# Kernel optimization log

Measured on AMD Instinct MI355X. Metric: run time of the kernel, lower is better.

Reference implementation:

```python
import jax, jax.numpy as jnp
import numpy as np

N, E, G = 50000, 800000, 256
H, C = 8, 16
F0 = 64
FH = H * C  # 128
L = 6
EPS = 1e-5
SEL = [0, 1, 2, 3, 4, 5, 5, 5]  # <10 layers -> pad with last


def setup_inputs() -> dict:
    key = jax.random.key(0)
    ks = jax.random.split(key, 32)

    def w(k, shape, fan_in):
        return jax.random.normal(k, shape, jnp.float32) / np.float32(np.sqrt(fan_in))

    inp = {
        'x': jax.random.normal(ks[0], (N, F0), jnp.float32),
        'edge_index': jax.random.randint(ks[1], (2, E), 0, N),
        'batch_vec': jnp.sort(jax.random.randint(ks[2], (N,), 0, G)),
        # layer 0 (in=F0)
        'Wq0': w(ks[3], (F0, FH), F0), 'bq0': 0.01 * jax.random.normal(ks[4], (FH,), jnp.float32),
        'Wk0': w(ks[5], (F0, FH), F0), 'bk0': 0.01 * jax.random.normal(ks[6], (FH,), jnp.float32),
        'Wv0': w(ks[7], (F0, FH), F0), 'bv0': 0.01 * jax.random.normal(ks[8], (FH,), jnp.float32),
        'Ws0': w(ks[9], (F0, FH), F0), 'bs0': 0.01 * jax.random.normal(ks[10], (FH,), jnp.float32),
        # layers 1..L-1 (in=FH), stacked
        'Wq': w(ks[11], (L - 1, FH, FH), FH), 'bq': 0.01 * jax.random.normal(ks[12], (L - 1, FH), jnp.float32),
        'Wk': w(ks[13], (L - 1, FH, FH), FH), 'bk': 0.01 * jax.random.normal(ks[14], (L - 1, FH), jnp.float32),
        'Wv': w(ks[15], (L - 1, FH, FH), FH), 'bv': 0.01 * jax.random.normal(ks[16], (L - 1, FH), jnp.float32),
        'Ws': w(ks[17], (L - 1, FH, FH), FH), 'bs': 0.01 * jax.random.normal(ks[18], (L - 1, FH), jnp.float32),
        # BatchNorm affine params per layer
        'gamma': jnp.ones((L, FH), jnp.float32),
        'beta': jnp.zeros((L, FH), jnp.float32),
    }
    return inp


def _transformer_conv(x, src, dst, Wq, bq, Wk, bk, Wv, bv, Ws, bs):
    # q from target nodes, k/v from source nodes (PyG TransformerConv, concat=True)
    q = (x @ Wq + bq).reshape(-1, H, C)
    k = (x @ Wk + bk).reshape(-1, H, C)
    v = (x @ Wv + bv).reshape(-1, H, C)
    s = jnp.einsum('ehc,ehc->eh', q[dst], k[src]) * np.float32(1.0 / np.sqrt(C))  # [E,H]
    m = jax.ops.segment_max(s, dst, num_segments=N)       # segment softmax over in-edges
    e = jnp.exp(s - m[dst])
    denom = jax.ops.segment_sum(e, dst, num_segments=N)
    alpha = e / jnp.maximum(denom[dst], 1e-16)            # [E,H]
    msg = jax.ops.segment_sum(alpha[:, :, None] * v[src], dst, num_segments=N)  # [N,H,C]
    return msg.reshape(-1, FH) + (x @ Ws + bs)            # root/skip connection


def _bn_relu(x, g, b):
    mu = jnp.mean(x, axis=0)
    var = jnp.var(x, axis=0)  # biased, as used for normalization in training mode
    return jax.nn.relu((x - mu) * jax.lax.rsqrt(var + EPS) * g + b)


def reference(x, edge_index, batch_vec, Wq0, bq0, Wk0, bk0, Wv0, bv0, Ws0, bs0,
              Wq, bq, Wk, bk, Wv, bv, Ws, bs, gamma, beta):
    src, dst = edge_index[0], edge_index[1]
    outs = []
    h = _bn_relu(_transformer_conv(x, src, dst, Wq0, bq0, Wk0, bk0, Wv0, bv0, Ws0, bs0),
                 gamma[0], beta[0])
    outs.append(h)
    for i in range(L - 1):
        h = _bn_relu(_transformer_conv(h, src, dst, Wq[i], bq[i], Wk[i], bk[i],
                                       Wv[i], bv[i], Ws[i], bs[i]),
                     gamma[i + 1], beta[i + 1])
        outs.append(h)
    counts = jnp.maximum(jax.ops.segment_sum(jnp.ones((N,), x.dtype), batch_vec, num_segments=G), 1.0)
    pooled = [jax.ops.segment_sum(o, batch_vec, num_segments=G) / counts[:, None] for o in outs]
    latent = jnp.stack([pooled[i] for i in SEL], axis=1)  # [G, 8, FH]
    return latent.reshape(G, -1)                          # [G, 8*FH]
```

## Files before the change

kernel.cpp:

```cpp
#include <hip/hip_runtime.h>
#include <hip/hip_bf16.h>
#include <math.h>

#define NN 50000
#define NE 800000
#define NG 256
#define FHH 128
#define NL 6
#define NCH 49
#define NB 391

typedef __attribute__((ext_vector_type(8))) short s16x8;
typedef __attribute__((ext_vector_type(4))) float f32x4;

#define QSCALE 0.36067376022224085f

__device__ __forceinline__ ushort f2bf(float x) {
  uint u = __float_as_uint(x);
  u += 0x7fffu + ((u >> 16) & 1u);
  return (ushort)(u >> 16);
}
__device__ __forceinline__ float bf2f(ushort h) {
  return __uint_as_float(((uint)h) << 16);
}
__device__ __forceinline__ float bfl(uint u) { return __uint_as_float(u << 16); }
__device__ __forceinline__ float bfh(uint u) { return __uint_as_float(u & 0xffff0000u); }
__device__ __forceinline__ uint packbf(float a, float b) {
  return (uint)f2bf(a) | ((uint)f2bf(b) << 16);
}

__device__ __forceinline__ void gload16(const ushort* g, ushort* l) {
  __builtin_amdgcn_global_load_lds(
      (const __attribute__((address_space(1))) uint*)(const void*)g,
      (__attribute__((address_space(3))) uint*)(void*)l, 16, 0, 0);
}

__global__ void k_gstart(const int* __restrict__ bv, int* __restrict__ gstart) {
  int g = blockIdx.x * blockDim.x + threadIdx.x;
  if (g > NG) return;
  int lo = 0, hi = NN;
  while (lo < hi) { int mid = (lo + hi) >> 1; if (bv[mid] < g) lo = mid + 1; else hi = mid; }
  gstart[g] = lo;
}

__global__ void k_deg(const int* __restrict__ dstv, int* __restrict__ deg) {
  int e = blockIdx.x * blockDim.x + threadIdx.x;
  if (e < NE) atomicAdd(&deg[dstv[e]], 1);
}

__global__ __launch_bounds__(256) void k_scanA(const int* __restrict__ deg, int* __restrict__ part) {
  int b = blockIdx.x, t = threadIdx.x;
  int s = 0;
  for (int j = t; j < 1024; j += 256) { int i = b * 1024 + j; if (i < NN) s += deg[i]; }
  __shared__ int sh[4];
  for (int o = 32; o; o >>= 1) s += __shfl_down(s, o, 64);
  if ((t & 63) == 0) sh[t >> 6] = s;
  __syncthreads();
  if (t == 0) part[b] = sh[0] + sh[1] + sh[2] + sh[3];
}

__global__ void k_scanB(int* __restrict__ part, int* __restrict__ row_ptr) {
  if (threadIdx.x == 0 && blockIdx.x == 0) {
    int run = 0;
    for (int i = 0; i < NCH; ++i) { int v = part[i]; part[i] = run; run += v; }
    row_ptr[NN] = run;
  }
}

__global__ __launch_bounds__(1024) void k_scanC(const int* __restrict__ deg, const int* __restrict__ part,
                                                int* __restrict__ row_ptr, int* __restrict__ cursor) {
  __shared__ int buf[1024];
  int b = blockIdx.x, t = threadIdx.x;
  int i = b * 1024 + t;
  int v = (i < NN) ? deg[i] : 0;
  buf[t] = v;
  __syncthreads();
  for (int off = 1; off < 1024; off <<= 1) {
    int add = (t >= off) ? buf[t - off] : 0;
    __syncthreads();
    buf[t] += add;
    __syncthreads();
  }
  if (i < NN) { int ex = part[b] + buf[t] - v; row_ptr[i] = ex; cursor[i] = ex; }
}

__global__ void k_scatter(const int* __restrict__ srcv, const int* __restrict__ dstv,
                          int* __restrict__ cursor, uint* __restrict__ colb) {
  int e = blockIdx.x * blockDim.x + threadIdx.x;
  if (e < NE) {
    int d = dstv[e];
    int pos = atomicAdd(&cursor[d], 1);
    colb[pos] = ((uint)srcv[e]) << 9;
  }
}

__device__ __forceinline__ size_t wtile_idx(int k, int c) {
  return (size_t)(k >> 5) * 4096 + ((((c >> 4) * 4 + ((k & 31) >> 3)) * 16 + (c & 15)) * 8 + (k & 7));
}

__global__ __launch_bounds__(256) void k_wconv0(const float* __restrict__ W0, const float* __restrict__ W1,
                                                const float* __restrict__ W2, const float* __restrict__ W3,
                                                ushort* __restrict__ wh, ushort* __restrict__ wl) {
  int id = blockIdx.x * 256 + threadIdx.x;
  if (id >= 4 * 64 * 128) return;
  int mat = id >> 13, rem = id & 8191;
  int k = rem >> 7, c = rem & 127;
  const float* W = (mat == 0) ? W0 : (mat == 1) ? W1 : (mat == 2) ? W2 : W3;
  float v = W[k * 128 + c];
  ushort h = f2bf(v);
  ushort lo = f2bf(v - bf2f(h));
  size_t dst = (size_t)mat * 8192 + wtile_idx(k, c);
  wh[dst] = h; wl[dst] = lo;
}

__global__ __launch_bounds__(256) void k_wconvS(const float* __restrict__ Wq, const float* __restrict__ Wk,
                                                const float* __restrict__ Wv, const float* __restrict__ Ws,
                                                ushort* __restrict__ wh, ushort* __restrict__ wl) {
  int id = blockIdx.x * 256 + threadIdx.x;
  if (id >= 5 * 4 * 16384) return;
  int lay = id / 65536, rem = id % 65536;
  int mat = rem >> 14, rem2 = rem & 16383;
  int k = rem2 >> 7, c = rem2 & 127;
  const float* W = (mat == 0) ? Wq : (mat == 1) ? Wk : (mat == 2) ? Wv : Ws;
  float v = W[(size_t)lay * 16384 + k * 128 + c];
  ushort h = f2bf(v);
  ushort lo = f2bf(v - bf2f(h));
  size_t dst = 32768 + ((size_t)lay * 4 + mat) * 16384 + wtile_idx(k, c);
  wh[dst] = h; wl[dst] = lo;
}

template <int K>
__global__ __launch_bounds__(256) void k_presplit(const float* __restrict__ Y,
                                                  ushort* __restrict__ Xh, ushort* __restrict__ Xl) {
  const int CP = K / 4;
  int idx = blockIdx.x * 256 + threadIdx.x;
  int row = idx / CP;
  int c4 = (idx % CP) * 4;
  if (row >= NN) return;
  float4 v = *reinterpret_cast<const float4*>(Y + (size_t)row * K + c4);
  ushort h0 = f2bf(v.x), h1 = f2bf(v.y), h2 = f2bf(v.z), h3 = f2bf(v.w);
  ushort l0 = f2bf(v.x - bf2f(h0)), l1 = f2bf(v.y - bf2f(h1));
  ushort l2 = f2bf(v.z - bf2f(h2)), l3 = f2bf(v.w - bf2f(h3));
  int b = row >> 7, g = (row & 127) >> 4, frow = row & 15;
  int ks = c4 >> 5, qq = (c4 & 31) >> 3, j = c4 & 7;
  size_t base = ((size_t)ks * NB + b) * 4096 + (((g * 4 + qq) * 16) + frow) * 8 + j;
  *reinterpret_cast<uint2*>(Xh + base) =
      make_uint2((uint)h0 | ((uint)h1 << 16), (uint)h2 | ((uint)h3 << 16));
  *reinterpret_cast<uint2*>(Xl + base) =
      make_uint2((uint)l0 | ((uint)l1 << 16), (uint)l2 | ((uint)l3 << 16));
}

template <int K>
__global__ __launch_bounds__(256, 2) void k_gemm(
    const ushort* __restrict__ Xh, const ushort* __restrict__ Xl,
    const ushort* __restrict__ Wth, const ushort* __restrict__ Wtl,
    const float* __restrict__ b0, const float* __restrict__ b1,
    const float* __restrict__ b2, const float* __restrict__ b3,
    ushort* __restrict__ qbf, ushort* __restrict__ kv, float* __restrict__ Yxs) {
  __shared__ __align__(16) ushort Ah[4096];
  __shared__ __align__(16) ushort Al[4096];
  __shared__ __align__(16) ushort Bh[4096];
  __shared__ __align__(16) ushort Bl[4096];
  int bid = blockIdx.x;
  int mat = (bid >> 3) & 3;
  int b = (bid & 7) + ((bid >> 5) << 3);
  if (b >= NB) return;
  int t = threadIdx.x;
  int lane = t & 63, w = t >> 6;
  int wr = w >> 1, wc = w & 1;
  int frow = lane & 15;
  const ushort* wh = Wth + (size_t)mat * (K * 128);
  const ushort* wl = Wtl + (size_t)mat * (K * 128);
  const float* bb = (mat == 0) ? b0 : (mat == 1) ? b1 : (mat == 2) ? b2 : b3;

  f32x4 acc[4][4];
#pragma unroll
  for (int i = 0; i < 4; ++i)
#pragma unroll
    for (int j = 0; j < 4; ++j)
#pragma unroll
      for (int r = 0; r < 4; ++r) acc[i][j][r] = 0.f;

  int wofs = w * 1024 + lane * 8;
  for (int ks = 0; ks < K / 32; ++ks) {
    size_t abase = ((size_t)ks * NB + b) * 4096;
    const ushort* gAh = Xh + abase + wofs;
    const ushort* gAl = Xl + abase + wofs;
    const ushort* gBh = wh + ks * 4096 + wofs;
    const ushort* gBl = wl + ks * 4096 + wofs;
    gload16(gAh, &Ah[w * 1024]);
    gload16(gAh + 512, &Ah[w * 1024 + 512]);
    gload16(gAl, &Al[w * 1024]);
    gload16(gAl + 512, &Al[w * 1024 + 512]);
    gload16(gBh, &Bh[w * 1024]);
    gload16(gBh + 512, &Bh[w * 1024 + 512]);
    gload16(gBl, &Bl[w * 1024]);
    gload16(gBl + 512, &Bl[w * 1024 + 512]);
    __syncthreads();
    s16x8 ah[4], al[4], bh[4], bl[4];
#pragma unroll
    for (int g = 0; g < 4; ++g) {
      ah[g] = *reinterpret_cast<const s16x8*>(&Ah[(wr * 4 + g) * 512 + lane * 8]);
      al[g] = *reinterpret_cast<const s16x8*>(&Al[(wr * 4 + g) * 512 + lane * 8]);
      bh[g] = *reinterpret_cast<const s16x8*>(&Bh[(wc * 4 + g) * 512 + lane * 8]);
      bl[g] = *reinterpret_cast<const s16x8*>(&Bl[(wc * 4 + g) * 512 + lane * 8]);
    }
#pragma unroll
    for (int rg = 0; rg < 4; ++rg)
#pragma unroll
      for (int cg = 0; cg < 4; ++cg) {
        acc[rg][cg] = __builtin_amdgcn_mfma_f32_16x16x32_bf16(ah[rg], bh[cg], acc[rg][cg], 0, 0, 0);
        acc[rg][cg] = __builtin_amdgcn_mfma_f32_16x16x32_bf16(al[rg], bh[cg], acc[rg][cg], 0, 0, 0);
        acc[rg][cg] = __builtin_amdgcn_mfma_f32_16x16x32_bf16(ah[rg], bl[cg], acc[rg][cg], 0, 0, 0);
      }
    __syncthreads();
  }
  int r0 = b * 128;
  int qq = (lane >> 4) << 2;
#pragma unroll
  for (int rg = 0; rg < 4; ++rg) {
#pragma unroll
    for (int cg = 0; cg < 4; ++cg) {
      int colg = wc * 64 + cg * 16 + frow;
      float bv = bb[colg];
#pragma unroll
      for (int r = 0; r < 4; ++r) {
        int row = r0 + wr * 64 + rg * 16 + qq + r;
        if (row >= NN) continue;
        float val = acc[rg][cg][r] + bv;
        if (mat == 0)      qbf[(size_t)row * FHH + colg] = f2bf(val * QSCALE);
        else if (mat == 3) Yxs[(size_t)row * FHH + colg] = val;
        else {
          int pos = (colg >> 1) * 4 + ((mat == 2) ? 2 : 0) + (colg & 1);
          kv[(size_t)row * 256 + pos] = f2bf(val);
        }
      }
    }
  }
}

__global__ __launch_bounds__(256) void k_agg(const uint* __restrict__ qb,
                                             const ushort* __restrict__ kv,
                                             const float* __restrict__ xs,
                                             const int* __restrict__ row_ptr,
                                             const uint* __restrict__ colb,
                                             uint* __restrict__ yb) {
  int n = blockIdx.x * 4 + (threadIdx.x >> 6);
  int t = threadIdx.x & 63;
  uint qp = qb[(n << 6) + t];
  float qx = bfl(qp), qy = bfh(qp);
  const char* kvb = (const char*)kv;
  uint tof = (uint)t * 8u;
  int e0 = row_ptr[n], e1 = row_ptr[n + 1];
  float sum = 0.f, a0 = 0.f, a1 = 0.f;
  int i = e0;
  for (; i + 4 <= e1; i += 4) {
    uint o0 = colb[i] + tof, o1 = colb[i + 1] + tof;
    uint o2 = colb[i + 2] + tof, o3 = colb[i + 3] + tof;
    uint2 d0 = *(const uint2*)(kvb + o0);
    uint2 d1 = *(const uint2*)(kvb + o1);
    uint2 d2 = *(const uint2*)(kvb + o2);
    uint2 d3 = *(const uint2*)(kvb + o3);
    float p0 = fmaf(qx, bfl(d0.x), qy * bfh(d0.x));
    float p1 = fmaf(qx, bfl(d1.x), qy * bfh(d1.x));
    float p2 = fmaf(qx, bfl(d2.x), qy * bfh(d2.x));
    float p3 = fmaf(qx, bfl(d3.x), qy * bfh(d3.x));
    p0 += __shfl_xor(p0, 1, 8); p1 += __shfl_xor(p1, 1, 8);
    p2 += __shfl_xor(p2, 1, 8); p3 += __shfl_xor(p3, 1, 8);
    p0 += __shfl_xor(p0, 2, 8); p1 += __shfl_xor(p1, 2, 8);
    p2 += __shfl_xor(p2, 2, 8); p3 += __shfl_xor(p3, 2, 8);
    p0 += __shfl_xor(p0, 4, 8); p1 += __shfl_xor(p1, 4, 8);
    p2 += __shfl_xor(p2, 4, 8); p3 += __shfl_xor(p3, 4, 8);
    float w0 = exp2f(fminf(p0, 110.f));
    float w1 = exp2f(fminf(p1, 110.f));
    float w2 = exp2f(fminf(p2, 110.f));
    float w3 = exp2f(fminf(p3, 110.f));
    sum += (w0 + w1) + (w2 + w3);
    a0 = fmaf(w0, bfl(d0.y), fmaf(w1, bfl(d1.y), fmaf(w2, bfl(d2.y), fmaf(w3, bfl(d3.y), a0))));
    a1 = fmaf(w0, bfh(d0.y), fmaf(w1, bfh(d1.y), fmaf(w2, bfh(d2.y), fmaf(w3, bfh(d3.y), a1))));
  }
  for (; i < e1; ++i) {
    uint o0 = colb[i] + tof;
    uint2 d0 = *(const uint2*)(kvb + o0);
    float p0 = fmaf(qx, bfl(d0.x), qy * bfh(d0.x));
    p0 += __shfl_xor(p0, 1, 8);
    p0 += __shfl_xor(p0, 2, 8);
    p0 += __shfl_xor(p0, 4, 8);
    float w0 = exp2f(fminf(p0, 110.f));
    sum += w0;
    a0 = fmaf(w0, bfl(d0.y), a0);
    a1 = fmaf(w0, bfh(d0.y), a1);
  }
  float inv = 1.f / fmaxf(sum, 1e-16f);
  float2 xv = *reinterpret_cast<const float2*>(xs + ((size_t)n << 7) + 2 * t);
  float ox = fmaf(a0, inv, xv.x);
  float oy = fmaf(a1, inv, xv.y);
  yb[(n << 6) + t] = packbf(ox, oy);
}

__global__ __launch_bounds__(256) void k_bnstats(const uint* __restrict__ yb,
                                                 float* __restrict__ stats) {
  __shared__ float2 s1[256], s2[256];
  int u = threadIdx.x & 63;
  int grp = threadIdx.x >> 6;
  float2 a = make_float2(0.f, 0.f), b = make_float2(0.f, 0.f);
  for (int r = blockIdx.x * 4 + grp; r < NN; r += 1024) {
    uint d = yb[(size_t)r * 64 + u];
    float x = bfl(d), yv = bfh(d);
    a.x += x; a.y += yv;
    b.x = fmaf(x, x, b.x); b.y = fmaf(yv, yv, b.y);
  }
  s1[threadIdx.x] = a;
  s2[threadIdx.x] = b;
  __syncthreads();
  if (grp == 0) {
#pragma unroll
    for (int g = 1; g < 4; ++g) {
      a.x += s1[u + 64 * g].x; a.y += s1[u + 64 * g].y;
      b.x += s2[u + 64 * g].x; b.y += s2[u + 64 * g].y;
    }
    atomicAdd(&stats[2 * u], a.x);
    atomicAdd(&stats[2 * u + 1], a.y);
    atomicAdd(&stats[128 + 2 * u], b.x);
    atomicAdd(&stats[128 + 2 * u + 1], b.y);
  }
}

template <int WRITE_X>
__global__ __launch_bounds__(256) void k_post(const uint* __restrict__ yb,
                                              const float* __restrict__ st,
                                              const float* __restrict__ gvec,
                                              const float* __restrict__ bvec_,
                                              const int* __restrict__ bv,
                                              const int* __restrict__ gstart,
                                              float* __restrict__ out, int layer,
                                              ushort* __restrict__ Xh, ushort* __restrict__ Xl) {
  __shared__ float acts[8][128];
  __shared__ int sg[8];
  __shared__ float ssc[128], ssh[128];
  int b = blockIdx.x, t = threadIdx.x;
  if (t < 128) {
    const float invn = 1.f / (float)NN;
    float mu = st[t] * invn;
    float var = st[128 + t] * invn - mu * mu;
    float sc = gvec[t] * rsqrtf(var + 1e-5f);
    ssc[t] = sc;
    ssh[t] = bvec_[t] - mu * sc;
  }
  if (t < 8) sg[t] = (b * 8 + t < NN) ? bv[b * 8 + t] : -1;
  __syncthreads();
  int row = b * 8 + (t >> 5);
  int c4 = (t & 31) * 4;
  bool ok = row < NN;
  float4 a = make_float4(0.f, 0.f, 0.f, 0.f);
  if (ok) {
    uint2 u2 = *reinterpret_cast<const uint2*>(yb + (size_t)row * 64 + (c4 >> 1));
    a.x = fmaxf(fmaf(bfl(u2.x), ssc[c4 + 0], ssh[c4 + 0]), 0.f);
    a.y = fmaxf(fmaf(bfh(u2.x), ssc[c4 + 1], ssh[c4 + 1]), 0.f);
    a.z = fmaxf(fmaf(bfl(u2.y), ssc[c4 + 2], ssh[c4 + 2]), 0.f);
    a.w = fmaxf(fmaf(bfh(u2.y), ssc[c4 + 3], ssh[c4 + 3]), 0.f);
  }
  *reinterpret_cast<float4*>(&acts[t >> 5][c4]) = a;
  if (WRITE_X && ok) {
    ushort h0 = f2bf(a.x), h1 = f2bf(a.y), h2 = f2bf(a.z), h3 = f2bf(a.w);
    ushort l0 = f2bf(a.x - bf2f(h0)), l1 = f2bf(a.y - bf2f(h1));
    ushort l2 = f2bf(a.z - bf2f(h2)), l3 = f2bf(a.w - bf2f(h3));
    int bb = row >> 7, g = (row & 127) >> 4, frow = row & 15;
    int ks = c4 >> 5, qq = (c4 & 31) >> 3, j = c4 & 7;
    size_t base = ((size_t)ks * NB + bb) * 4096 + (((g * 4 + qq) * 16) + frow) * 8 + j;
    *reinterpret_cast<uint2*>(Xh + base) =
        make_uint2((uint)h0 | ((uint)h1 << 16), (uint)h2 | ((uint)h3 << 16));
    *reinterpret_cast<uint2*>(Xl + base) =
        make_uint2((uint)l0 | ((uint)l1 << 16), (uint)l2 | ((uint)l3 << 16));
  }
  __syncthreads();
  if (t < 128) {
    float racc = 0.f;
    int cg = sg[0];
    for (int r = 0; r < 8; ++r) {
      int g = sg[r];
      if (g != cg) {
        if (cg >= 0) {
          float p = racc / (float)(gstart[cg + 1] - gstart[cg]);
          if (layer < 5) atomicAdd(&out[(size_t)cg * 1024 + layer * FHH + t], p);
          else {
            atomicAdd(&out[(size_t)cg * 1024 + 5 * FHH + t], p);
            atomicAdd(&out[(size_t)cg * 1024 + 6 * FHH + t], p);
            atomicAdd(&out[(size_t)cg * 1024 + 7 * FHH + t], p);
          }
        }
        racc = 0.f;
        cg = g;
      }
      racc += acts[r][t];
    }
    if (cg >= 0) {
      float p = racc / (float)(gstart[cg + 1] - gstart[cg]);
      if (layer < 5) atomicAdd(&out[(size_t)cg * 1024 + layer * FHH + t], p);
      else {
        atomicAdd(&out[(size_t)cg * 1024 + 5 * FHH + t], p);
        atomicAdd(&out[(size_t)cg * 1024 + 6 * FHH + t], p);
        atomicAdd(&out[(size_t)cg * 1024 + 7 * FHH + t], p);
      }
    }
  }
}

extern "C" void kernel_launch(void* const* d_in, const int* in_sizes, int n_in,
                              void* d_out, int out_size, void* d_ws, size_t ws_size,
                              hipStream_t stream) {
  (void)in_sizes; (void)n_in; (void)ws_size;
  const float* x    = (const float*)d_in[0];
  const int*   ei   = (const int*)d_in[1];
  const int*   bvec = (const int*)d_in[2];
  const float* Wq0  = (const float*)d_in[3];
  const float* bq0  = (const float*)d_in[4];
  const float* Wk0  = (const float*)d_in[5];
  const float* bk0  = (const float*)d_in[6];
  const float* Wv0  = (const float*)d_in[7];
  const float* bv0  = (const float*)d_in[8];
  const float* Ws0  = (const float*)d_in[9];
  const float* bs0  = (const float*)d_in[10];
  const float* WqS  = (const float*)d_in[11];
  const float* bqS  = (const float*)d_in[12];
  const float* WkS  = (const float*)d_in[13];
  const float* bkS  = (const float*)d_in[14];
  const float* WvS  = (const float*)d_in[15];
  const float* bvS  = (const float*)d_in[16];
  const float* WsS  = (const float*)d_in[17];
  const float* bsS  = (const float*)d_in[18];
  const float* gamma = (const float*)d_in[19];
  const float* beta  = (const float*)d_in[20];
  float* out = (float*)d_out;

  char* ws = (char*)d_ws;
  size_t off = 0;
  auto alloc = [&](size_t bytes) {
    void* p = ws + off;
    off = (off + bytes + 255) & ~(size_t)255;
    return p;
  };
  ushort* qbf = (ushort*)alloc((size_t)NN * FHH * 2);
  float* xs   = (float*)alloc((size_t)NN * FHH * 4);
  uint* yb    = (uint*)alloc((size_t)NN * 64 * 4);
  ushort* kv  = (ushort*)alloc((size_t)NN * 256 * 2);
  ushort* Xh  = (ushort*)alloc((size_t)4 * NB * 4096 * 2 + 8192);
  ushort* Xl  = (ushort*)alloc((size_t)4 * NB * 4096 * 2 + 8192);
  uint* colb   = (uint*)alloc((size_t)NE * 4);
  int* row_ptr = (int*)alloc((size_t)(NN + 1) * 4);
  int* cursor  = (int*)alloc((size_t)NN * 4);
  int* deg     = (int*)alloc((size_t)NN * 4);
  int* part    = (int*)alloc((size_t)NCH * 4);
  int* gstart  = (int*)alloc((size_t)(NG + 1) * 4);
  float* bstat = (float*)alloc((size_t)NL * 2 * FHH * 4);
  ushort* wsh = (ushort*)alloc((size_t)360448 * 2);
  ushort* wsl = (ushort*)alloc((size_t)360448 * 2);

  const int* srcv = ei;
  const int* dstv = ei + NE;

  hipMemsetAsync(out, 0, (size_t)out_size * 4, stream);
  hipMemsetAsync(deg, 0, (size_t)NN * 4, stream);
  hipMemsetAsync(bstat, 0, (size_t)NL * 2 * FHH * 4, stream);
  k_gstart<<<5, 64, 0, stream>>>(bvec, gstart);
  k_deg<<<(NE + 255) / 256, 256, 0, stream>>>(dstv, deg);
  k_scanA<<<NCH, 256, 0, stream>>>(deg, part);
  k_scanB<<<1, 64, 0, stream>>>(part, row_ptr);
  k_scanC<<<NCH, 1024, 0, stream>>>(deg, part, row_ptr, cursor);
  k_scatter<<<(NE + 255) / 256, 256, 0, stream>>>(srcv, dstv, cursor, colb);
  k_wconv0<<<128, 256, 0, stream>>>(Wq0, Wk0, Wv0, Ws0, wsh, wsl);
  k_wconvS<<<1280, 256, 0, stream>>>(WqS, WkS, WvS, WsS, wsh, wsl);
  k_presplit<64><<<(NN * 16 + 255) / 256, 256, 0, stream>>>(x, Xh, Xl);

  const int GEMM_GRID = 49 * 32;
  for (int l = 0; l < NL; ++l) {
    const ushort* WthL = wsh + ((l == 0) ? 0 : (size_t)32768 + (size_t)(l - 1) * 65536);
    const ushort* WtlL = wsl + ((l == 0) ? 0 : (size_t)32768 + (size_t)(l - 1) * 65536);
    const float *bq_, *bk_, *bv_, *bs_;
    if (l == 0) { bq_ = bq0; bk_ = bk0; bv_ = bv0; bs_ = bs0; }
    else {
      size_t bo = (size_t)(l - 1) * FHH;
      bq_ = bqS + bo; bk_ = bkS + bo; bv_ = bvS + bo; bs_ = bsS + bo;
    }
    if (l == 0)
      k_gemm<64><<<GEMM_GRID, 256, 0, stream>>>(Xh, Xl, WthL, WtlL, bq_, bk_, bv_, bs_, qbf, kv, xs);
    else
      k_gemm<128><<<GEMM_GRID, 256, 0, stream>>>(Xh, Xl, WthL, WtlL, bq_, bk_, bv_, bs_, qbf, kv, xs);
    k_agg<<<NN / 4, 256, 0, stream>>>((const uint*)qbf, kv, xs, row_ptr, colb, yb);
    float* lstat = bstat + (size_t)l * 2 * FHH;
    k_bnstats<<<256, 256, 0, stream>>>(yb, lstat);
    if (l + 1 < NL)
      k_post<1><<<6250, 256, 0, stream>>>(yb, lstat, gamma + (size_t)l * FHH,
                                          beta + (size_t)l * FHH, bvec, gstart, out, l, Xh, Xl);
    else
      k_post<0><<<6250, 256, 0, stream>>>(yb, lstat, gamma + (size_t)l * FHH,
                                          beta + (size_t)l * FHH, bvec, gstart, out, l, Xh, Xl);
  }
}
```

Before: 950.8 us.

## Widen aggregation gathers to 16 bytes per lane and store skip output as bf16

The aggregation kernel now has each lane handle four feature channels using 16-byte gathers. Each wavefront half processes a different edge, and the two halves are combined with a cross-half shuffle at the end. Per-edge shuffle reduction depth drops from three to two steps, and a bf16 dot2 intrinsic is used when available. The skip/root projection output is stored as bf16 instead of fp32, which halves that buffer's traffic at some cost in precision.

```diff
diff --git a/kernel.cpp b/kernel.cpp
--- a/kernel.cpp
+++ b/kernel.cpp
@@ -15,6 +15,15 @@
 
 #define QSCALE 0.36067376022224085f
 
+#if defined(__has_builtin)
+#if __has_builtin(__builtin_amdgcn_fdot2_f32_bf16)
+#define HAVE_BFDOT 1
+#endif
+#endif
+#ifndef HAVE_BFDOT
+#define HAVE_BFDOT 0
+#endif
+
 __device__ __forceinline__ ushort f2bf(float x) {
   uint u = __float_as_uint(x);
   u += 0x7fffu + ((u >> 16) & 1u);
@@ -28,6 +37,14 @@
 __device__ __forceinline__ uint packbf(float a, float b) {
   return (uint)f2bf(a) | ((uint)f2bf(b) << 16);
 }
+
+#if HAVE_BFDOT
+typedef __attribute__((ext_vector_type(2))) __bf16 bf16v2;
+__device__ __forceinline__ float dot2acc(uint a, uint b, float acc) {
+  return __builtin_amdgcn_fdot2_f32_bf16(__builtin_bit_cast(bf16v2, a),
+                                         __builtin_bit_cast(bf16v2, b), acc, false);
+}
+#endif
 
 __device__ __forceinline__ void gload16(const ushort* g, ushort* l) {
   __builtin_amdgcn_global_load_lds(
@@ -156,7 +173,7 @@
     const ushort* __restrict__ Wth, const ushort* __restrict__ Wtl,
     const float* __restrict__ b0, const float* __restrict__ b1,
     const float* __restrict__ b2, const float* __restrict__ b3,
-    ushort* __restrict__ qbf, ushort* __restrict__ kv, float* __restrict__ Yxs) {
+    ushort* __restrict__ qbf, ushort* __restrict__ kv, ushort* __restrict__ xsb) {
   __shared__ __align__(16) ushort Ah[4096];
   __shared__ __align__(16) ushort Al[4096];
   __shared__ __align__(16) ushort Bh[4096];
@@ -229,7 +246,7 @@
         if (row >= NN) continue;
         float val = acc[rg][cg][r] + bv;
         if (mat == 0)      qbf[(size_t)row * FHH + colg] = f2bf(val * QSCALE);
-        else if (mat == 3) Yxs[(size_t)row * FHH + colg] = val;
+        else if (mat == 3) xsb[(size_t)row * FHH + colg] = f2bf(val);
         else {
           int pos = (colg >> 1) * 4 + ((mat == 2) ? 2 : 0) + (colg & 1);
           kv[(size_t)row * 256 + pos] = f2bf(val);
@@ -241,61 +258,108 @@
 
 __global__ __launch_bounds__(256) void k_agg(const uint* __restrict__ qb,
                                              const ushort* __restrict__ kv,
-                                             const float* __restrict__ xs,
+                                             const uint* __restrict__ xsb,
                                              const int* __restrict__ row_ptr,
                                              const uint* __restrict__ colb,
                                              uint* __restrict__ yb) {
   int n = blockIdx.x * 4 + (threadIdx.x >> 6);
-  int t = threadIdx.x & 63;
-  uint qp = qb[(n << 6) + t];
-  float qx = bfl(qp), qy = bfh(qp);
+  int lane = threadIdx.x & 63;
+  int hl = lane & 31, half = lane >> 5;
+  uint2 qp = *reinterpret_cast<const uint2*>(qb + (n << 6) + 2 * hl);
+#if !HAVE_BFDOT
+  float qa = bfl(qp.x), qbv = bfh(qp.x), qc = bfl(qp.y), qd = bfh(qp.y);
+#endif
   const char* kvb = (const char*)kv;
-  uint tof = (uint)t * 8u;
+  uint tof = (uint)hl * 16u;
   int e0 = row_ptr[n], e1 = row_ptr[n + 1];
-  float sum = 0.f, a0 = 0.f, a1 = 0.f;
+  float sum = 0.f, a0 = 0.f, a1 = 0.f, a2 = 0.f, a3 = 0.f;
   int i = e0;
   for (; i + 4 <= e1; i += 4) {
-    uint o0 = colb[i] + tof, o1 = colb[i + 1] + tof;
-    uint o2 = colb[i + 2] + tof, o3 = colb[i + 3] + tof;
-    uint2 d0 = *(const uint2*)(kvb + o0);
-    uint2 d1 = *(const uint2*)(kvb + o1);
-    uint2 d2 = *(const uint2*)(kvb + o2);
-    uint2 d3 = *(const uint2*)(kvb + o3);
-    float p0 = fmaf(qx, bfl(d0.x), qy * bfh(d0.x));
-    float p1 = fmaf(qx, bfl(d1.x), qy * bfh(d1.x));
-    float p2 = fmaf(qx, bfl(d2.x), qy * bfh(d2.x));
-    float p3 = fmaf(qx, bfl(d3.x), qy * bfh(d3.x));
-    p0 += __shfl_xor(p0, 1, 8); p1 += __shfl_xor(p1, 1, 8);
-    p2 += __shfl_xor(p2, 1, 8); p3 += __shfl_xor(p3, 1, 8);
-    p0 += __shfl_xor(p0, 2, 8); p1 += __shfl_xor(p1, 2, 8);
-    p2 += __shfl_xor(p2, 2, 8); p3 += __shfl_xor(p3, 2, 8);
-    p0 += __shfl_xor(p0, 4, 8); p1 += __shfl_xor(p1, 4, 8);
-    p2 += __shfl_xor(p2, 4, 8); p3 += __shfl_xor(p3, 4, 8);
-    float w0 = exp2f(fminf(p0, 110.f));
-    float w1 = exp2f(fminf(p1, 110.f));
-    float w2 = exp2f(fminf(p2, 110.f));
-    float w3 = exp2f(fminf(p3, 110.f));
-    sum += (w0 + w1) + (w2 + w3);
-    a0 = fmaf(w0, bfl(d0.y), fmaf(w1, bfl(d1.y), fmaf(w2, bfl(d2.y), fmaf(w3, bfl(d3.y), a0))));
-    a1 = fmaf(w0, bfh(d0.y), fmaf(w1, bfh(d1.y), fmaf(w2, bfh(d2.y), fmaf(w3, bfh(d3.y), a1))));
-  }
-  for (; i < e1; ++i) {
-    uint o0 = colb[i] + tof;
-    uint2 d0 = *(const uint2*)(kvb + o0);
-    float p0 = fmaf(qx, bfl(d0.x), qy * bfh(d0.x));
-    p0 += __shfl_xor(p0, 1, 8);
-    p0 += __shfl_xor(p0, 2, 8);
-    p0 += __shfl_xor(p0, 4, 8);
-    float w0 = exp2f(fminf(p0, 110.f));
-    sum += w0;
-    a0 = fmaf(w0, bfl(d0.y), a0);
-    a1 = fmaf(w0, bfh(d0.y), a1);
-  }
+    uint oA = colb[i + half] + tof;
+    uint oB = colb[i + 2 + half] + tof;
+    uint4 dA = *(const uint4*)(kvb + oA);
+    uint4 dB = *(const uint4*)(kvb + oB);
+#if HAVE_BFDOT
+    float pA = dot2acc(dA.z, qp.y, dot2acc(dA.x, qp.x, 0.f));
+    float pB = dot2acc(dB.z, qp.y, dot2acc(dB.x, qp.x, 0.f));
+#else
+    float pA = qa * bfl(dA.x);
+    pA = fmaf(qbv, bfh(dA.x), pA);
+    pA = fmaf(qc, bfl(dA.z), pA);
+    pA = fmaf(qd, bfh(dA.z), pA);
+    float pB = qa * bfl(dB.x);
+    pB = fmaf(qbv, bfh(dB.x), pB);
+    pB = fmaf(qc, bfl(dB.z), pB);
+    pB = fmaf(qd, bfh(dB.z), pB);
+#endif
+    pA += __shfl_xor(pA, 1, 4);  pB += __shfl_xor(pB, 1, 4);
+    pA += __shfl_xor(pA, 2, 4);  pB += __shfl_xor(pB, 2, 4);
+    float wA = exp2f(fminf(pA, 110.f));
+    float wB = exp2f(fminf(pB, 110.f));
+    sum += wA + wB;
+    a0 = fmaf(wA, bfl(dA.y), fmaf(wB, bfl(dB.y), a0));
+    a1 = fmaf(wA, bfh(dA.y), fmaf(wB, bfh(dB.y), a1));
+    a2 = fmaf(wA, bfl(dA.w), fmaf(wB, bfl(dB.w), a2));
+    a3 = fmaf(wA, bfh(dA.w), fmaf(wB, bfh(dB.w), a3));
+  }
+  for (; i + 2 <= e1; i += 2) {
+    uint oA = colb[i + half] + tof;
+    uint4 dA = *(const uint4*)(kvb + oA);
+#if HAVE_BFDOT
+    float pA = dot2acc(dA.z, qp.y, dot2acc(dA.x, qp.x, 0.f));
+#else
+    float pA = qa * bfl(dA.x);
+    pA = fmaf(qbv, bfh(dA.x), pA);
+    pA = fmaf(qc, bfl(dA.z), pA);
+    pA = fmaf(qd, bfh(dA.z), pA);
+#endif
+    pA += __shfl_xor(pA, 1, 4);
+    pA += __shfl_xor(pA, 2, 4);
+    float wA = exp2f(fminf(pA, 110.f));
+    sum += wA;
+    a0 = fmaf(wA, bfl(dA.y), a0);
+    a1 = fmaf(wA, bfh(dA.y), a1);
+    a2 = fmaf(wA, bfl(dA.w), a2);
+    a3 = fmaf(wA, bfh(dA.w), a3);
+  }
+  if (i < e1) {
+    uint oA = colb[i] + tof;
+    uint4 dA = *(const uint4*)(kvb + oA);
+#if HAVE_BFDOT
+    float pA = dot2acc(dA.z, qp.y, dot2acc(dA.x, qp.x, 0.f));
+#else
+    float pA = qa * bfl(dA.x);
+    pA = fmaf(qbv, bfh(dA.x), pA);
+    pA = fmaf(qc, bfl(dA.z), pA);
+    pA = fmaf(qd, bfh(dA.z), pA);
+#endif
+    pA += __shfl_xor(pA, 1, 4);
+    pA += __shfl_xor(pA, 2, 4);
+    float wA = exp2f(fminf(pA, 110.f));
+    if (half) wA = 0.f;
+    sum += wA;
+    a0 = fmaf(wA, bfl(dA.y), a0);
+    a1 = fmaf(wA, bfh(dA.y), a1);
+    a2 = fmaf(wA, bfl(dA.w), a2);
+    a3 = fmaf(wA, bfh(dA.w), a3);
+  }
+  sum += __shfl_xor(sum, 32);
+  a0 += __shfl_xor(a0, 32);
+  a1 += __shfl_xor(a1, 32);
+  a2 += __shfl_xor(a2, 32);
+  a3 += __shfl_xor(a3, 32);
   float inv = 1.f / fmaxf(sum, 1e-16f);
-  float2 xv = *reinterpret_cast<const float2*>(xs + ((size_t)n << 7) + 2 * t);
-  float ox = fmaf(a0, inv, xv.x);
-  float oy = fmaf(a1, inv, xv.y);
-  yb[(n << 6) + t] = packbf(ox, oy);
+  uint2 xv = *reinterpret_cast<const uint2*>(xsb + (n << 6) + 2 * hl);
+  float o0 = fmaf(a0, inv, bfl(xv.x));
+  float o1 = fmaf(a1, inv, bfh(xv.x));
+  float o2 = fmaf(a2, inv, bfl(xv.y));
+  float o3 = fmaf(a3, inv, bfh(xv.y));
+  if (half == 0) {
+    uint2 o;
+    o.x = packbf(o0, o1);
+    o.y = packbf(o2, o3);
+    *reinterpret_cast<uint2*>(yb + (n << 6) + 2 * hl) = o;
+  }
 }
 
 __global__ __launch_bounds__(256) void k_bnstats(const uint* __restrict__ yb,
@@ -441,7 +505,7 @@
     return p;
   };
   ushort* qbf = (ushort*)alloc((size_t)NN * FHH * 2);
-  float* xs   = (float*)alloc((size_t)NN * FHH * 4);
+  ushort* xsb = (ushort*)alloc((size_t)NN * FHH * 2);
   uint* yb    = (uint*)alloc((size_t)NN * 64 * 4);
   ushort* kv  = (ushort*)alloc((size_t)NN * 256 * 2);
   ushort* Xh  = (ushort*)alloc((size_t)4 * NB * 4096 * 2 + 8192);
@@ -483,10 +547,10 @@
       bq_ = bqS + bo; bk_ = bkS + bo; bv_ = bvS + bo; bs_ = bsS + bo;
     }
     if (l == 0)
-      k_gemm<64><<<GEMM_GRID, 256, 0, stream>>>(Xh, Xl, WthL, WtlL, bq_, bk_, bv_, bs_, qbf, kv, xs);
+      k_gemm<64><<<GEMM_GRID, 256, 0, stream>>>(Xh, Xl, WthL, WtlL, bq_, bk_, bv_, bs_, qbf, kv, xsb);
     else
-      k_gemm<128><<<GEMM_GRID, 256, 0, stream>>>(Xh, Xl, WthL, WtlL, bq_, bk_, bv_, bs_, qbf, kv, xs);
-    k_agg<<<NN / 4, 256, 0, stream>>>((const uint*)qbf, kv, xs, row_ptr, colb, yb);
+      k_gemm<128><<<GEMM_GRID, 256, 0, stream>>>(Xh, Xl, WthL, WtlL, bq_, bk_, bv_, bs_, qbf, kv, xsb);
+    k_agg<<<NN / 4, 256, 0, stream>>>((const uint*)qbf, kv, (const uint*)xsb, row_ptr, colb, yb);
     float* lstat = bstat + (size_t)l * 2 * FHH;
     k_bnstats<<<256, 256, 0, stream>>>(yb, lstat);
     if (l + 1 < NL)
```

Measured after the change: 941.4 us. About the same (-1.0%).
